# Performance work log

Measured on AMD Instinct MI355X. Metric: run time of the kernel, lower is better.

## Reference

```python
import jax, jax.numpy as jnp
import numpy as np

EPS = 1e-5
B, C, T = 128, 64, 1000          # batch, EEG channels, time samples
NCLU, HID, NOUT = 8, 512, 4      # clusters, head hidden dim, outputs (=feature_dim)


def _conv1d(x, w):
    # x: (N, Cin, T), w: (Cout, Cin, K), valid conv along time
    return jax.lax.conv_general_dilated(x, w, (1,), 'VALID',
                                        dimension_numbers=('NCH', 'OIH', 'NCH'))


def _bn(x, g, b, m, v):
    # eval-mode BatchNorm over channel dim of (N, C, T)
    return (x - m[None, :, None]) * (g / jnp.sqrt(v + EPS))[None, :, None] + b[None, :, None]


def _pool3(x):
    # maxpool kernel 3 stride 3 along time
    return jax.lax.reduce_window(x, -jnp.inf, jax.lax.max, (1, 1, 3), (1, 1, 3), 'VALID')


def setup_inputs() -> dict:
    key = jax.random.key(0)
    ks = jax.random.split(key, 12)
    def nrm(k, shape, fan):
        return jax.random.normal(k, shape, jnp.float32) / np.float32(np.sqrt(fan))
    inp = {
        'x': jax.random.normal(ks[0], (B, C, T), jnp.float32),
        'cluster_ids': jax.random.randint(ks[1], (B,), 0, NCLU, jnp.int32),
        # Deep4Net-style backbone params
        'w_time': nrm(ks[2], (25, 1, 10), 10),
        'b_time': jnp.zeros((25,), jnp.float32),
        'w_spat': nrm(ks[3], (25, 25, C), 25 * C),
        'w2': nrm(ks[4], (50, 25, 10), 250),
        'w3': nrm(ks[5], (100, 50, 10), 500),
        'w4': nrm(ks[6], (200, 100, 10), 1000),
        'w_cls': nrm(ks[7], (NOUT, 200, 7), 1400),
        'b_cls': jnp.zeros((NOUT,), jnp.float32),
        # per-cluster expert head params
        'hW1': nrm(ks[8], (NCLU, HID, NOUT), NOUT),
        'hb1': jnp.zeros((NCLU, HID), jnp.float32),
        'hW2': nrm(ks[9], (NCLU, NOUT, HID), HID),
        'hb2': jnp.zeros((NCLU, NOUT), jnp.float32),
        'hg': jnp.ones((NCLU, HID), jnp.float32),
        'hbe': jnp.zeros((NCLU, HID), jnp.float32),
        'hm': jnp.zeros((NCLU, HID), jnp.float32),
        'hv': jnp.ones((NCLU, HID), jnp.float32),
    }
    for i, c in zip((1, 2, 3, 4), (25, 50, 100, 200)):
        inp[f'g{i}'] = jnp.ones((c,), jnp.float32)
        inp[f'be{i}'] = jnp.zeros((c,), jnp.float32)
        inp[f'm{i}'] = jnp.zeros((c,), jnp.float32)
        inp[f'v{i}'] = jnp.ones((c,), jnp.float32)
    return inp


def reference(x, cluster_ids, w_time, b_time, w_spat, w2, w3, w4, w_cls, b_cls,
              hW1, hb1, hW2, hb2, hg, hbe, hm, hv,
              g1, be1, m1, v1, g2, be2, m2, v2, g3, be3, m3, v3, g4, be4, m4, v4):
    b_, c_, t_ = x.shape
    # conv_time: same 25 temporal filters applied per EEG channel -> (B, C, 25, T1)
    h = _conv1d(x.reshape(b_ * c_, 1, t_), w_time) + b_time[None, :, None]
    h = h.reshape(b_, c_, 25, -1)
    # conv_spat: collapse EEG channel axis -> (B, 25, T1)
    z = jnp.einsum('bcft,gfc->bgt', h, w_spat)
    z = _pool3(jax.nn.elu(_bn(z, g1, be1, m1, v1)))
    for w, g, be, m, v in ((w2, g2, be2, m2, v2), (w3, g3, be3, m3, v3), (w4, g4, be4, m4, v4)):
        z = _pool3(jax.nn.elu(_bn(_conv1d(z, w), g, be, m, v)))
    # final_conv_length='auto': classifier conv reduces time dim to 1 -> (B, NOUT)
    feats = (_conv1d(z, w_cls) + b_cls[None, :, None])[:, :, 0]
    # per-sample expert head routing (Linear -> BN(eval) -> ReLU -> [Dropout eval] -> Linear)
    h1 = jnp.einsum('bf,bhf->bh', feats, hW1[cluster_ids]) + hb1[cluster_ids]
    h1 = (h1 - hm[cluster_ids]) * (hg[cluster_ids] / jnp.sqrt(hv[cluster_ids] + EPS)) + hbe[cluster_ids]
    h1 = jax.nn.relu(h1)
    return jnp.einsum('bh,boh->bo', h1, hW2[cluster_ids]) + hb2[cluster_ids]
```

## Files before the change

kernel.cpp:

```cpp
#include <hip/hip_runtime.h>
#include <math.h>

#define EPS_BN 1e-5f

typedef __attribute__((ext_vector_type(8))) short short8;
typedef __attribute__((ext_vector_type(4))) float f32x4;
typedef __attribute__((ext_vector_type(4))) unsigned int uint4v;

__device__ __forceinline__ unsigned short f2bf(float f) {
    unsigned int u = __float_as_uint(f);
    u = (u + 0x7fffu + ((u >> 16) & 1u)) >> 16;
    return (unsigned short)u;
}
__device__ __forceinline__ float bf2f(unsigned short s) {
    return __uint_as_float(((unsigned int)s) << 16);
}
__device__ __forceinline__ float elu1(float y) { return y > 0.f ? y : expm1f(y); }
__device__ __forceinline__ float warp_sum(float v) {
    for (int off = 32; off > 0; off >>= 1) v += __shfl_down(v, off);
    return v;
}

#define UW1 0
#define UW2 20480
#define UW3 40960
#define UW4 122880
#define BB1 0
#define BB2 32
#define BB3 96
#define BB4 224
#define XTG_U 410496
#define Z1G_U 9192320
#define Z2G_U 10544000
#define Z3G_U 11420544

#define NPREP 1602
#define RS_ZB 36

__global__ __launch_bounds__(256) void kprep_tr(
    const float* __restrict__ x,
    const float* __restrict__ w_time, const float* __restrict__ b_time,
    const float* __restrict__ w_spat,
    const float* __restrict__ w2, const float* __restrict__ w3,
    const float* __restrict__ w4,
    const float* __restrict__ g1, const float* __restrict__ be1,
    const float* __restrict__ m1, const float* __restrict__ v1,
    const float* __restrict__ g2, const float* __restrict__ be2,
    const float* __restrict__ m2, const float* __restrict__ v2,
    const float* __restrict__ g3, const float* __restrict__ be3,
    const float* __restrict__ m3, const float* __restrict__ v3,
    const float* __restrict__ g4, const float* __restrict__ be4,
    const float* __restrict__ m4, const float* __restrict__ v4,
    unsigned short* __restrict__ wsz, float* __restrict__ biasf) {
    __shared__ float tr[64 * 65];
    if (blockIdx.x < NPREP) {
        int idx = blockIdx.x * 256 + threadIdx.x;
        if (idx < 20480) {
            int k = idx >> 11, g = (idx >> 6) & 31, c = idx & 63;
            float val = 0.f;
            if (g < 25) {
                float s = 0.f;
#pragma unroll
                for (int f = 0; f < 25; ++f)
                    s = fmaf(w_spat[g * 1600 + f * 64 + c], w_time[f * 10 + k], s);
                val = s * (g1[g] * rsqrtf(v1[g] + EPS_BN));
            }
            wsz[UW1 + idx] = f2bf(val);
        } else if (idx < 40960) {
            int j = idx - 20480;
            int k = j >> 11, g = (j >> 5) & 63, c = j & 31;
            float val = 0.f;
            if (g < 50 && c < 25)
                val = w2[(g * 25 + c) * 10 + k] * (g2[g] * rsqrtf(v2[g] + EPS_BN));
            wsz[UW2 + j] = f2bf(val);
        } else if (idx < 122880) {
            int j = idx - 40960;
            int k = j >> 13, g = (j >> 6) & 127, c = j & 63;
            float val = 0.f;
            if (g < 100 && c < 50)
                val = w3[(g * 50 + c) * 10 + k] * (g3[g] * rsqrtf(v3[g] + EPS_BN));
            wsz[UW3 + j] = f2bf(val);
        } else if (idx < 409600) {
            int j = idx - 122880;
            int k = j / 28672, r = j % 28672, g = r >> 7, c = r & 127;
            float val = 0.f;
            if (g < 200 && c < 100)
                val = w4[(g * 100 + c) * 10 + k] * (g4[g] * rsqrtf(v4[g] + EPS_BN));
            wsz[UW4 + j] = f2bf(val);
        } else if (idx < 410048) {
            int j = idx - 409600;
            if (j < 32) {
                int g = j; float val = 0.f;
                if (g < 25) {
                    float beff = 0.f;
                    for (int f = 0; f < 25; ++f) {
                        float a = 0.f;
                        for (int c = 0; c < 64; ++c) a += w_spat[g * 1600 + f * 64 + c];
                        beff = fmaf(a, b_time[f], beff);
                    }
                    float sc = g1[g] * rsqrtf(v1[g] + EPS_BN);
                    val = be1[g] - m1[g] * sc + beff * sc;
                }
                biasf[BB1 + g] = val;
            } else if (j < 96) {
                int g = j - 32; float val = 0.f;
                if (g < 50) { float sc = g2[g] * rsqrtf(v2[g] + EPS_BN); val = be2[g] - m2[g] * sc; }
                biasf[BB2 + g] = val;
            } else if (j < 224) {
                int g = j - 96; float val = 0.f;
                if (g < 100) { float sc = g3[g] * rsqrtf(v3[g] + EPS_BN); val = be3[g] - m3[g] * sc; }
                biasf[BB3 + g] = val;
            } else {
                int g = j - 224; float val = 0.f;
                if (g < 200) { float sc = g4[g] * rsqrtf(v4[g] + EPS_BN); val = be4[g] - m4[g] * sc; }
                biasf[BB4 + g] = val;
            }
        }
    } else {
        const int bid = blockIdx.x - NPREP;
        const int b = bid / 17, tile = bid % 17, t = threadIdx.x;
        const int t0 = tile * 64;
        const float* xb = x + b * 64000;
        for (int idx = t; idx < 1024; idx += 256) {
            int c = idx >> 4, q = idx & 15;
            int tg = t0 + 4 * q;
            float4 v = {0.f, 0.f, 0.f, 0.f};
            if (tg + 4 <= 1000) {
                v = *(const float4*)(xb + c * 1000 + tg);
            } else {
                float* pv = (float*)&v;
#pragma unroll
                for (int e = 0; e < 4; ++e)
                    if (tg + e < 1000) pv[e] = xb[c * 1000 + tg + e];
            }
            tr[c * 65 + 4 * q]     = v.x;
            tr[c * 65 + 4 * q + 1] = v.y;
            tr[c * 65 + 4 * q + 2] = v.z;
            tr[c * 65 + 4 * q + 3] = v.w;
        }
        __syncthreads();
        unsigned short* xTg = wsz + XTG_U;
        for (int idx = t; idx < 2048; idx += 256) {
            int tl = idx >> 5, cp = idx & 31;
            int tg = t0 + tl;
            unsigned int pk = 0u;
            if (tg < 1000)
                pk = (unsigned int)f2bf(tr[(2 * cp) * 65 + tl]) |
                     ((unsigned int)f2bf(tr[(2 * cp + 1) * 65 + tl]) << 16);
            if (tg < 1072)
                *(unsigned int*)&xTg[(b * 1072 + tg) * 64 + 2 * cp] = pk;
        }
    }
}

template<int CPAD, int RS, int SP, int TT, int TPC, int NCHUNK, int JMAX,
         int GPAD, int TPOOL, int GSTORE, int NGV, int OUT_RS, bool OUT_F32,
         int KPRE>
__device__ __forceinline__ void conv_job(
    const unsigned short* xT, const unsigned short* __restrict__ wpk,
    const float* __restrict__ bias,
    unsigned short* zout, float* zoutf, unsigned short* zbw,
    int lane, int gbi, int po0) {
    const int lm = lane & 15, h8 = lane >> 4;
    const int gloc = lane & 31, hh = lane >> 5;

    f32x4 acc[TT][2];
#pragma unroll
    for (int i = 0; i < TT; ++i) {
        acc[i][0] = (f32x4){0.f, 0.f, 0.f, 0.f};
        acc[i][1] = (f32x4){0.f, 0.f, 0.f, 0.f};
    }

    const int abase = lm * RS + h8 * 8;
    const unsigned short* wp = wpk + (gbi * 32 + lm) * CPAD + h8 * 8;
#pragma unroll
    for (int ph = 0; ph < 10 / KPRE; ++ph) {
        short8 w0r[KPRE][SP], w1r[KPRE][SP];
#pragma unroll
        for (int kk = 0; kk < KPRE; ++kk) {
            const int k = ph * KPRE + kk;
#pragma unroll
            for (int s = 0; s < SP; ++s) {
                w0r[kk][s] = *(const short8*)(wp + k * (GPAD * CPAD) + s * 32);
                w1r[kk][s] = *(const short8*)(wp + k * (GPAD * CPAD) + 16 * CPAD + s * 32);
            }
        }
#pragma unroll
        for (int kk = 0; kk < KPRE; ++kk) {
            const int k = ph * KPRE + kk;
#pragma unroll
            for (int s = 0; s < SP; ++s) {
#pragma unroll
                for (int tt = 0; tt < TT; ++tt) {
                    short8 a = *(const short8*)&xT[abase + (tt * 16 + k) * RS + s * 32];
                    acc[tt][0] = __builtin_amdgcn_mfma_f32_16x16x32_bf16(
                        a, w0r[kk][s], acc[tt][0], 0, 0, 0);
                    acc[tt][1] = __builtin_amdgcn_mfma_f32_16x16x32_bf16(
                        a, w1r[kk][s], acc[tt][1], 0, 0, 0);
                }
            }
        }
    }

    const float bv0 = bias[gbi * 32 + lm];
    const float bv1 = bias[gbi * 32 + 16 + lm];
#pragma unroll
    for (int ch = 0; ch < NCHUNK; ++ch) {
#pragma unroll
        for (int ti = 0; ti < TPC; ++ti) {
            int ttg = ch * TPC + ti;
#pragma unroll
            for (int r = 0; r < 4; ++r) {
                float v0 = elu1(acc[ttg][0][r] + bv0);
                float v1 = elu1(acc[ttg][1][r] + bv1);
                int row = ti * 16 + 4 * h8 + r;
                zbw[row * RS_ZB + lm] = f2bf(v0);
                zbw[row * RS_ZB + 16 + lm] = f2bf(v1);
            }
        }
#pragma unroll
        for (int j = 0; j < JMAX; ++j) {
            int po = hh + 2 * j;
            if (3 * po + 2 < TPC * 16) {
                float q0 = bf2f(zbw[(3 * po) * RS_ZB + gloc]);
                float q1 = bf2f(zbw[(3 * po + 1) * RS_ZB + gloc]);
                float q2 = bf2f(zbw[(3 * po + 2) * RS_ZB + gloc]);
                float mx = fmaxf(q0, fmaxf(q1, q2));
                int poa = po0 + ch * 16 + po;
                int ga = gbi * 32 + gloc;
                if (poa < TPOOL && ga < GSTORE) {
                    if constexpr (OUT_F32)
                        zoutf[poa * OUT_RS + ga] = mx;
                    else
                        zout[poa * OUT_RS + ga] =
                            (ga < NGV) ? f2bf(mx) : (unsigned short)0;
                }
            }
        }
    }
}

__global__ __launch_bounds__(64) void ks1(
    const unsigned short* __restrict__ wsu, const float* __restrict__ biasf,
    unsigned short* __restrict__ wsz) {
    __shared__ __align__(16) unsigned short xT[64 * 72];
    __shared__ __align__(16) unsigned short zb[48 * RS_ZB];
    const int b = blockIdx.x, tci = blockIdx.y, lane = threadIdx.x;
    const unsigned short* xTg = wsz + XTG_U + (b * 1072 + tci * 48) * 64;
    for (int idx = lane; idx < 512; idx += 64) {
        int r = idx >> 3, q = idx & 7;
        *(uint4v*)&xT[r * 72 + 8 * q] = *(const uint4v*)&xTg[r * 64 + 8 * q];
    }
    __syncthreads();
    conv_job<64, 72, 2, 3, 3, 1, 8, 32, 330, 32, 25, 32, false, 5>(
        xT, wsu + UW1, biasf + BB1,
        wsz + Z1G_U + b * 330 * 32, nullptr, zb, lane, 0, tci * 16);
}

__global__ __launch_bounds__(64) void ks2(
    const unsigned short* __restrict__ wsu, const float* __restrict__ biasf,
    unsigned short* __restrict__ wsz) {
    __shared__ __align__(16) unsigned short xT[64 * 40];
    __shared__ __align__(16) unsigned short zb[48 * RS_ZB];
    const int b = blockIdx.x, y = blockIdx.y, lane = threadIdx.x;
    const int gbi = y / 7, tci = y % 7, t0b = tci * 48;
    const unsigned short* z1g = wsz + Z1G_U + b * 330 * 32;
    for (int idx = lane; idx < 256; idx += 64) {
        int r = idx >> 2, q = idx & 3;
        uint4v v = {0u, 0u, 0u, 0u};
        if (t0b + r < 330) v = *(const uint4v*)&z1g[(t0b + r) * 32 + 8 * q];
        *(uint4v*)&xT[r * 40 + 8 * q] = v;
    }
    __syncthreads();
    conv_job<32, 40, 1, 3, 3, 1, 8, 64, 107, 64, 50, 64, false, 5>(
        xT, wsu + UW2, biasf + BB2,
        wsz + Z2G_U + b * 107 * 64, nullptr, zb, lane, gbi, tci * 16);
}

__global__ __launch_bounds__(64) void ks3(
    const unsigned short* __restrict__ wsu, const float* __restrict__ biasf,
    unsigned short* __restrict__ wsz) {
    __shared__ __align__(16) unsigned short z2t[64 * 72];
    __shared__ __align__(16) unsigned short zb[48 * RS_ZB];
    const int b = blockIdx.x, y = blockIdx.y, lane = threadIdx.x;
    const int gbi = y / 2, tci = y % 2, t0b = tci * 48;
    const unsigned short* z2g = wsz + Z2G_U + b * 107 * 64;
    for (int idx = lane; idx < 512; idx += 64) {
        int r = idx >> 3, q = idx & 7;
        uint4v v = {0u, 0u, 0u, 0u};
        if (t0b + r < 107) v = *(const uint4v*)&z2g[(t0b + r) * 64 + 8 * q];
        *(uint4v*)&z2t[r * 72 + 8 * q] = v;
    }
    __syncthreads();
    conv_job<64, 72, 2, 3, 3, 1, 8, 128, 32, 128, 100, 136, false, 5>(
        z2t, wsu + UW3, biasf + BB3,
        wsz + Z3G_U + b * 44 * 136, nullptr, zb, lane, gbi, tci * 16);
}

__global__ __launch_bounds__(448) void ks4h(
    const unsigned short* __restrict__ wsu, const float* __restrict__ biasf,
    const unsigned short* __restrict__ wsz,
    const float* __restrict__ w_cls, const float* __restrict__ b_cls,
    const int* __restrict__ cid,
    const float* __restrict__ hW1, const float* __restrict__ hb1,
    const float* __restrict__ hW2, const float* __restrict__ hb2,
    const float* __restrict__ hg, const float* __restrict__ hbe,
    const float* __restrict__ hm, const float* __restrict__ hv,
    float* __restrict__ out) {
    __shared__ __align__(16) unsigned short z3t[44 * 136];
    __shared__ __align__(16) unsigned short zb[7 * 32 * RS_ZB];
    __shared__ float z4f[1400];
    __shared__ float feats[4];
    __shared__ float h1s[512];
    const int b = blockIdx.x, t = threadIdx.x;
    const int lane = t & 63, wv = t >> 6;
    const unsigned short* z3g = wsz + Z3G_U + b * 44 * 136;
    for (int idx = t; idx < 748; idx += 448) {
        int r = idx / 17, q = idx % 17;
        uint4v v = {0u, 0u, 0u, 0u};
        if (r < 32) v = *(const uint4v*)&z3g[r * 136 + 8 * q];
        *(uint4v*)&z3t[r * 136 + 8 * q] = v;
    }
    __syncthreads();

    conv_job<128, 136, 4, 2, 2, 1, 4, 224, 7, 200, 200, 200, true, 5>(
        z3t, wsu + UW4, biasf + BB4,
        nullptr, z4f, zb + wv * (32 * RS_ZB), lane, wv, 0);
    __syncthreads();

    if (wv < 4) {
        float p = 0.f;
        for (int i = lane; i < 1400; i += 64) {
            int po = i / 200, g = i - po * 200;
            p = fmaf(z4f[i], w_cls[wv * 1400 + g * 7 + po], p);
        }
        p = warp_sum(p);
        if (lane == 0) feats[wv] = p + b_cls[wv];
    }
    __syncthreads();

    const int c = cid[b];
    const float f0 = feats[0], f1 = feats[1], f2 = feats[2], f3 = feats[3];
    for (int h = t; h < 512; h += 448) {
        const float* w1 = &hW1[(c * 512 + h) * 4];
        float v = f0 * w1[0] + f1 * w1[1] + f2 * w1[2] + f3 * w1[3] + hb1[c * 512 + h];
        float sc = hg[c * 512 + h] * rsqrtf(hv[c * 512 + h] + EPS_BN);
        v = (v - hm[c * 512 + h]) * sc + hbe[c * 512 + h];
        h1s[h] = fmaxf(v, 0.f);
    }
    __syncthreads();
    if (wv < 4) {
        float p = 0.f;
        for (int i = lane; i < 512; i += 64)
            p = fmaf(h1s[i], hW2[(c * 4 + wv) * 512 + i], p);
        p = warp_sum(p);
        if (lane == 0) out[b * 4 + wv] = p + hb2[c * 4 + wv];
    }
}

extern "C" void kernel_launch(void* const* d_in, const int* in_sizes, int n_in,
                              void* d_out, int out_size, void* d_ws, size_t ws_size,
                              hipStream_t stream) {
    const float* x      = (const float*)d_in[0];
    const int*   cid    = (const int*)d_in[1];
    const float* w_time = (const float*)d_in[2];
    const float* b_time = (const float*)d_in[3];
    const float* w_spat = (const float*)d_in[4];
    const float* w2     = (const float*)d_in[5];
    const float* w3     = (const float*)d_in[6];
    const float* w4     = (const float*)d_in[7];
    const float* w_cls  = (const float*)d_in[8];
    const float* b_cls  = (const float*)d_in[9];
    const float* hW1    = (const float*)d_in[10];
    const float* hb1    = (const float*)d_in[11];
    const float* hW2    = (const float*)d_in[12];
    const float* hb2    = (const float*)d_in[13];
    const float* hg     = (const float*)d_in[14];
    const float* hbe    = (const float*)d_in[15];
    const float* hm     = (const float*)d_in[16];
    const float* hv     = (const float*)d_in[17];
    const float* g1  = (const float*)d_in[18];
    const float* be1 = (const float*)d_in[19];
    const float* m1  = (const float*)d_in[20];
    const float* v1  = (const float*)d_in[21];
    const float* g2  = (const float*)d_in[22];
    const float* be2 = (const float*)d_in[23];
    const float* m2  = (const float*)d_in[24];
    const float* v2  = (const float*)d_in[25];
    const float* g3  = (const float*)d_in[26];
    const float* be3 = (const float*)d_in[27];
    const float* m3  = (const float*)d_in[28];
    const float* v3  = (const float*)d_in[29];
    const float* g4  = (const float*)d_in[30];
    const float* be4 = (const float*)d_in[31];
    const float* m4  = (const float*)d_in[32];
    const float* v4  = (const float*)d_in[33];

    unsigned short* wsz = (unsigned short*)d_ws;
    float* biasf = (float*)((char*)d_ws + 819200);
    float* out = (float*)d_out;

    kprep_tr<<<NPREP + 128 * 17, 256, 0, stream>>>(
        x, w_time, b_time, w_spat, w2, w3, w4,
        g1, be1, m1, v1, g2, be2, m2, v2, g3, be3, m3, v3, g4, be4, m4, v4,
        wsz, biasf);

    ks1<<<dim3(128, 21), 64, 0, stream>>>(wsz, biasf, wsz);
    ks2<<<dim3(128, 14), 64, 0, stream>>>(wsz, biasf, wsz);
    ks3<<<dim3(128, 8), 64, 0, stream>>>(wsz, biasf, wsz);
    ks4h<<<128, 448, 0, stream>>>(wsz, biasf, wsz, w_cls, b_cls, cid,
                                  hW1, hb1, hW2, hb2, hg, hbe, hm, hv, out);
}
```

Before: 104.9 us.

## Split conv jobs into 16-channel waves and separate layer-4 conv from head

Each wave now computes 16 output channels instead of 32, and several waves share one staged input tile per block. This raises the number of waves in flight and cuts the redundant loads of the same input tile. Layer 4 moves out of the fused head kernel into its own 13-column grid that writes fp32 activations to the workspace, and a separate head kernel reads them back. This adds one kernel launch and a global round trip, and each wave now issues half as many MFMAs per A-fragment load.

```diff
diff --git a/kernel.cpp b/kernel.cpp
--- a/kernel.cpp
+++ b/kernel.cpp
@@ -33,9 +33,11 @@
 #define Z1G_U 9192320
 #define Z2G_U 10544000
 #define Z3G_U 11420544
+#define Z4G_BYTE 24372992
 
 #define NPREP 1602
-#define RS_ZB 36
+#define RS2 20
+#define ZBW (48 * RS2)
 
 __global__ __launch_bounds__(256) void kprep_tr(
     const float* __restrict__ x,
@@ -153,37 +155,31 @@
     }
 }
 
-template<int CPAD, int RS, int SP, int TT, int TPC, int NCHUNK, int JMAX,
+template<int CPAD, int RS, int SP, int TT, int TPC, int JMAX4,
          int GPAD, int TPOOL, int GSTORE, int NGV, int OUT_RS, bool OUT_F32,
          int KPRE>
-__device__ __forceinline__ void conv_job(
+__device__ __forceinline__ void conv_job16(
     const unsigned short* xT, const unsigned short* __restrict__ wpk,
     const float* __restrict__ bias,
     unsigned short* zout, float* zoutf, unsigned short* zbw,
-    int lane, int gbi, int po0) {
+    int lane, int gh, int po0) {
     const int lm = lane & 15, h8 = lane >> 4;
-    const int gloc = lane & 31, hh = lane >> 5;
-
-    f32x4 acc[TT][2];
-#pragma unroll
-    for (int i = 0; i < TT; ++i) {
-        acc[i][0] = (f32x4){0.f, 0.f, 0.f, 0.f};
-        acc[i][1] = (f32x4){0.f, 0.f, 0.f, 0.f};
-    }
+
+    f32x4 acc[TT];
+#pragma unroll
+    for (int i = 0; i < TT; ++i) acc[i] = (f32x4){0.f, 0.f, 0.f, 0.f};
 
     const int abase = lm * RS + h8 * 8;
-    const unsigned short* wp = wpk + (gbi * 32 + lm) * CPAD + h8 * 8;
+    const unsigned short* wp = wpk + (gh * 16 + lm) * CPAD + h8 * 8;
 #pragma unroll
     for (int ph = 0; ph < 10 / KPRE; ++ph) {
-        short8 w0r[KPRE][SP], w1r[KPRE][SP];
+        short8 w0r[KPRE][SP];
 #pragma unroll
         for (int kk = 0; kk < KPRE; ++kk) {
             const int k = ph * KPRE + kk;
 #pragma unroll
-            for (int s = 0; s < SP; ++s) {
+            for (int s = 0; s < SP; ++s)
                 w0r[kk][s] = *(const short8*)(wp + k * (GPAD * CPAD) + s * 32);
-                w1r[kk][s] = *(const short8*)(wp + k * (GPAD * CPAD) + 16 * CPAD + s * 32);
-            }
         }
 #pragma unroll
         for (int kk = 0; kk < KPRE; ++kk) {
@@ -193,113 +189,133 @@
 #pragma unroll
                 for (int tt = 0; tt < TT; ++tt) {
                     short8 a = *(const short8*)&xT[abase + (tt * 16 + k) * RS + s * 32];
-                    acc[tt][0] = __builtin_amdgcn_mfma_f32_16x16x32_bf16(
-                        a, w0r[kk][s], acc[tt][0], 0, 0, 0);
-                    acc[tt][1] = __builtin_amdgcn_mfma_f32_16x16x32_bf16(
-                        a, w1r[kk][s], acc[tt][1], 0, 0, 0);
+                    acc[tt] = __builtin_amdgcn_mfma_f32_16x16x32_bf16(
+                        a, w0r[kk][s], acc[tt], 0, 0, 0);
                 }
             }
         }
     }
 
-    const float bv0 = bias[gbi * 32 + lm];
-    const float bv1 = bias[gbi * 32 + 16 + lm];
-#pragma unroll
-    for (int ch = 0; ch < NCHUNK; ++ch) {
-#pragma unroll
-        for (int ti = 0; ti < TPC; ++ti) {
-            int ttg = ch * TPC + ti;
-#pragma unroll
-            for (int r = 0; r < 4; ++r) {
-                float v0 = elu1(acc[ttg][0][r] + bv0);
-                float v1 = elu1(acc[ttg][1][r] + bv1);
-                int row = ti * 16 + 4 * h8 + r;
-                zbw[row * RS_ZB + lm] = f2bf(v0);
-                zbw[row * RS_ZB + 16 + lm] = f2bf(v1);
+    const float bv0 = bias[gh * 16 + lm];
+#pragma unroll
+    for (int ti = 0; ti < TPC; ++ti) {
+#pragma unroll
+        for (int r = 0; r < 4; ++r) {
+            float v0 = elu1(acc[ti][r] + bv0);
+            int row = ti * 16 + 4 * h8 + r;
+            zbw[row * RS2 + lm] = f2bf(v0);
+        }
+    }
+#pragma unroll
+    for (int j = 0; j < JMAX4; ++j) {
+        int po = h8 + 4 * j;
+        if (3 * po + 2 < TPC * 16) {
+            float q0 = bf2f(zbw[(3 * po) * RS2 + lm]);
+            float q1 = bf2f(zbw[(3 * po + 1) * RS2 + lm]);
+            float q2 = bf2f(zbw[(3 * po + 2) * RS2 + lm]);
+            float mx = fmaxf(q0, fmaxf(q1, q2));
+            int poa = po0 + po;
+            int ga = gh * 16 + lm;
+            if (poa < TPOOL && ga < GSTORE) {
+                if constexpr (OUT_F32)
+                    zoutf[poa * OUT_RS + ga] = mx;
+                else
+                    zout[poa * OUT_RS + ga] =
+                        (ga < NGV) ? f2bf(mx) : (unsigned short)0;
             }
         }
-#pragma unroll
-        for (int j = 0; j < JMAX; ++j) {
-            int po = hh + 2 * j;
-            if (3 * po + 2 < TPC * 16) {
-                float q0 = bf2f(zbw[(3 * po) * RS_ZB + gloc]);
-                float q1 = bf2f(zbw[(3 * po + 1) * RS_ZB + gloc]);
-                float q2 = bf2f(zbw[(3 * po + 2) * RS_ZB + gloc]);
-                float mx = fmaxf(q0, fmaxf(q1, q2));
-                int poa = po0 + ch * 16 + po;
-                int ga = gbi * 32 + gloc;
-                if (poa < TPOOL && ga < GSTORE) {
-                    if constexpr (OUT_F32)
-                        zoutf[poa * OUT_RS + ga] = mx;
-                    else
-                        zout[poa * OUT_RS + ga] =
-                            (ga < NGV) ? f2bf(mx) : (unsigned short)0;
-                }
-            }
-        }
-    }
-}
-
-__global__ __launch_bounds__(64) void ks1(
+    }
+}
+
+__global__ __launch_bounds__(256) void ks1(
     const unsigned short* __restrict__ wsu, const float* __restrict__ biasf,
     unsigned short* __restrict__ wsz) {
-    __shared__ __align__(16) unsigned short xT[64 * 72];
-    __shared__ __align__(16) unsigned short zb[48 * RS_ZB];
-    const int b = blockIdx.x, tci = blockIdx.y, lane = threadIdx.x;
-    const unsigned short* xTg = wsz + XTG_U + (b * 1072 + tci * 48) * 64;
-    for (int idx = lane; idx < 512; idx += 64) {
+    __shared__ __align__(16) unsigned short xT[112 * 72];
+    __shared__ __align__(16) unsigned short zb[4 * ZBW];
+    const int b = blockIdx.x, by = blockIdx.y, t = threadIdx.x;
+    const int lane = t & 63, wv = t >> 6;
+    const int t0 = by * 96;
+    const unsigned short* xTg = wsz + XTG_U + (b * 1072 + t0) * 64;
+    for (int idx = t; idx < 112 * 8; idx += 256) {
         int r = idx >> 3, q = idx & 7;
         *(uint4v*)&xT[r * 72 + 8 * q] = *(const uint4v*)&xTg[r * 64 + 8 * q];
     }
     __syncthreads();
-    conv_job<64, 72, 2, 3, 3, 1, 8, 32, 330, 32, 25, 32, false, 5>(
-        xT, wsu + UW1, biasf + BB1,
-        wsz + Z1G_U + b * 330 * 32, nullptr, zb, lane, 0, tci * 16);
-}
-
-__global__ __launch_bounds__(64) void ks2(
+    const int tc = wv & 1, gh = wv >> 1;
+    const int tci = 2 * by + tc;
+    if (tci < 21) {
+        conv_job16<64, 72, 2, 3, 3, 4, 32, 330, 32, 25, 32, false, 5>(
+            xT + (tc * 48) * 72, wsu + UW1, biasf + BB1,
+            wsz + Z1G_U + b * 330 * 32, nullptr, zb + wv * ZBW,
+            lane, gh, tci * 16);
+    }
+}
+
+__global__ __launch_bounds__(256) void ks2(
     const unsigned short* __restrict__ wsu, const float* __restrict__ biasf,
     unsigned short* __restrict__ wsz) {
     __shared__ __align__(16) unsigned short xT[64 * 40];
-    __shared__ __align__(16) unsigned short zb[48 * RS_ZB];
-    const int b = blockIdx.x, y = blockIdx.y, lane = threadIdx.x;
-    const int gbi = y / 7, tci = y % 7, t0b = tci * 48;
+    __shared__ __align__(16) unsigned short zb[4 * ZBW];
+    const int b = blockIdx.x, tci = blockIdx.y, t = threadIdx.x;
+    const int lane = t & 63, wv = t >> 6;
+    const int t0b = tci * 48;
     const unsigned short* z1g = wsz + Z1G_U + b * 330 * 32;
-    for (int idx = lane; idx < 256; idx += 64) {
+    for (int idx = t; idx < 256; idx += 256) {
         int r = idx >> 2, q = idx & 3;
         uint4v v = {0u, 0u, 0u, 0u};
         if (t0b + r < 330) v = *(const uint4v*)&z1g[(t0b + r) * 32 + 8 * q];
         *(uint4v*)&xT[r * 40 + 8 * q] = v;
     }
     __syncthreads();
-    conv_job<32, 40, 1, 3, 3, 1, 8, 64, 107, 64, 50, 64, false, 5>(
+    conv_job16<32, 40, 1, 3, 3, 4, 64, 107, 64, 50, 64, false, 5>(
         xT, wsu + UW2, biasf + BB2,
-        wsz + Z2G_U + b * 107 * 64, nullptr, zb, lane, gbi, tci * 16);
-}
-
-__global__ __launch_bounds__(64) void ks3(
+        wsz + Z2G_U + b * 107 * 64, nullptr, zb + wv * ZBW,
+        lane, wv, tci * 16);
+}
+
+__global__ __launch_bounds__(512) void ks3(
     const unsigned short* __restrict__ wsu, const float* __restrict__ biasf,
     unsigned short* __restrict__ wsz) {
     __shared__ __align__(16) unsigned short z2t[64 * 72];
-    __shared__ __align__(16) unsigned short zb[48 * RS_ZB];
-    const int b = blockIdx.x, y = blockIdx.y, lane = threadIdx.x;
-    const int gbi = y / 2, tci = y % 2, t0b = tci * 48;
+    __shared__ __align__(16) unsigned short zb[8 * ZBW];
+    const int b = blockIdx.x, tci = blockIdx.y, t = threadIdx.x;
+    const int lane = t & 63, wv = t >> 6;
+    const int t0b = tci * 48;
     const unsigned short* z2g = wsz + Z2G_U + b * 107 * 64;
-    for (int idx = lane; idx < 512; idx += 64) {
+    for (int idx = t; idx < 512; idx += 512) {
         int r = idx >> 3, q = idx & 7;
         uint4v v = {0u, 0u, 0u, 0u};
         if (t0b + r < 107) v = *(const uint4v*)&z2g[(t0b + r) * 64 + 8 * q];
         *(uint4v*)&z2t[r * 72 + 8 * q] = v;
     }
     __syncthreads();
-    conv_job<64, 72, 2, 3, 3, 1, 8, 128, 32, 128, 100, 136, false, 5>(
+    conv_job16<64, 72, 2, 3, 3, 4, 128, 32, 128, 100, 136, false, 5>(
         z2t, wsu + UW3, biasf + BB3,
-        wsz + Z3G_U + b * 44 * 136, nullptr, zb, lane, gbi, tci * 16);
-}
-
-__global__ __launch_bounds__(448) void ks4h(
+        wsz + Z3G_U + b * 44 * 136, nullptr, zb + wv * ZBW,
+        lane, wv, tci * 16);
+}
+
+__global__ __launch_bounds__(64) void ks4(
     const unsigned short* __restrict__ wsu, const float* __restrict__ biasf,
-    const unsigned short* __restrict__ wsz,
+    unsigned short* __restrict__ wsz, float* __restrict__ z4g) {
+    __shared__ __align__(16) unsigned short z3t[44 * 136];
+    __shared__ __align__(16) unsigned short zb[ZBW];
+    const int b = blockIdx.x, gh = blockIdx.y, lane = threadIdx.x;
+    const unsigned short* z3g = wsz + Z3G_U + b * 44 * 136;
+    for (int idx = lane; idx < 748; idx += 64) {
+        int r = idx / 17, q = idx % 17;
+        uint4v v = {0u, 0u, 0u, 0u};
+        if (r < 32) v = *(const uint4v*)&z3g[r * 136 + 8 * q];
+        *(uint4v*)&z3t[r * 136 + 8 * q] = v;
+    }
+    __syncthreads();
+    conv_job16<128, 136, 4, 2, 2, 2, 224, 7, 200, 200, 200, true, 5>(
+        z3t, wsu + UW4, biasf + BB4,
+        nullptr, z4g + b * 1400, zb, lane, gh, 0);
+}
+
+__global__ __launch_bounds__(256) void kh(
+    const float* __restrict__ z4g,
     const float* __restrict__ w_cls, const float* __restrict__ b_cls,
     const int* __restrict__ cid,
     const float* __restrict__ hW1, const float* __restrict__ hb1,
@@ -307,28 +323,15 @@
     const float* __restrict__ hg, const float* __restrict__ hbe,
     const float* __restrict__ hm, const float* __restrict__ hv,
     float* __restrict__ out) {
-    __shared__ __align__(16) unsigned short z3t[44 * 136];
-    __shared__ __align__(16) unsigned short zb[7 * 32 * RS_ZB];
     __shared__ float z4f[1400];
     __shared__ float feats[4];
     __shared__ float h1s[512];
     const int b = blockIdx.x, t = threadIdx.x;
-    const int lane = t & 63, wv = t >> 6;
-    const unsigned short* z3g = wsz + Z3G_U + b * 44 * 136;
-    for (int idx = t; idx < 748; idx += 448) {
-        int r = idx / 17, q = idx % 17;
-        uint4v v = {0u, 0u, 0u, 0u};
-        if (r < 32) v = *(const uint4v*)&z3g[r * 136 + 8 * q];
-        *(uint4v*)&z3t[r * 136 + 8 * q] = v;
-    }
-    __syncthreads();
-
-    conv_job<128, 136, 4, 2, 2, 1, 4, 224, 7, 200, 200, 200, true, 5>(
-        z3t, wsu + UW4, biasf + BB4,
-        nullptr, z4f, zb + wv * (32 * RS_ZB), lane, wv, 0);
-    __syncthreads();
-
-    if (wv < 4) {
+    for (int i = t; i < 1400; i += 256) z4f[i] = z4g[b * 1400 + i];
+    __syncthreads();
+
+    const int wv = t >> 6, lane = t & 63;
+    {
         float p = 0.f;
         for (int i = lane; i < 1400; i += 64) {
             int po = i / 200, g = i - po * 200;
@@ -341,7 +344,7 @@
 
     const int c = cid[b];
     const float f0 = feats[0], f1 = feats[1], f2 = feats[2], f3 = feats[3];
-    for (int h = t; h < 512; h += 448) {
+    for (int h = t; h < 512; h += 256) {
         const float* w1 = &hW1[(c * 512 + h) * 4];
         float v = f0 * w1[0] + f1 * w1[1] + f2 * w1[2] + f3 * w1[3] + hb1[c * 512 + h];
         float sc = hg[c * 512 + h] * rsqrtf(hv[c * 512 + h] + EPS_BN);
@@ -349,7 +352,7 @@
         h1s[h] = fmaxf(v, 0.f);
     }
     __syncthreads();
-    if (wv < 4) {
+    {
         float p = 0.f;
         for (int i = lane; i < 512; i += 64)
             p = fmaf(h1s[i], hW2[(c * 4 + wv) * 512 + i], p);
@@ -398,6 +401,7 @@
 
     unsigned short* wsz = (unsigned short*)d_ws;
     float* biasf = (float*)((char*)d_ws + 819200);
+    float* z4g   = (float*)((char*)d_ws + Z4G_BYTE);
     float* out = (float*)d_out;
 
     kprep_tr<<<NPREP + 128 * 17, 256, 0, stream>>>(
@@ -405,9 +409,10 @@
         g1, be1, m1, v1, g2, be2, m2, v2, g3, be3, m3, v3, g4, be4, m4, v4,
         wsz, biasf);
 
-    ks1<<<dim3(128, 21), 64, 0, stream>>>(wsz, biasf, wsz);
-    ks2<<<dim3(128, 14), 64, 0, stream>>>(wsz, biasf, wsz);
-    ks3<<<dim3(128, 8), 64, 0, stream>>>(wsz, biasf, wsz);
-    ks4h<<<128, 448, 0, stream>>>(wsz, biasf, wsz, w_cls, b_cls, cid,
-                                  hW1, hb1, hW2, hb2, hg, hbe, hm, hv, out);
-}
+    ks1<<<dim3(128, 11), 256, 0, stream>>>(wsz, biasf, wsz);
+    ks2<<<dim3(128, 7), 256, 0, stream>>>(wsz, biasf, wsz);
+    ks3<<<dim3(128, 2), 512, 0, stream>>>(wsz, biasf, wsz);
+    ks4<<<dim3(128, 13), 64, 0, stream>>>(wsz, biasf, wsz, z4g);
+    kh<<<128, 256, 0, stream>>>(z4g, w_cls, b_cls, cid, hW1, hb1, hW2, hb2,
+                                hg, hbe, hm, hv, out);
+}
```

Result: faster. 94.12 us (-10.3%).
